# Kernel optimization log

Measured on AMD Instinct MI355X. Metric: run time of the kernel, lower is better.

Reference implementation:

```python
import jax, jax.numpy as jnp
import numpy as np

BETA = 1.0 - 0.01      # 1 - voltage_decay
THRESH = 1.0           # threshold_voltage; theta state is never updated in the
                       # original forward (theta1/theta2 stay at init=0), so the
                       # effective adaptive threshold is THRESH + 0 every step.
ALPHA = 2.0            # snntorch default ATan surrogate alpha

@jax.custom_vjp
def spike_fn(x):
    # Heaviside forward, ATan surrogate backward (snntorch default spike_grad)
    return (x > 0).astype(x.dtype)

def _spike_fwd(x):
    return (x > 0).astype(x.dtype), x

def _spike_bwd(x, g):
    return (g * (ALPHA / 2.0) / (1.0 + (jnp.pi / 2.0 * ALPHA * x) ** 2),)

spike_fn.defvjp(_spike_fwd, _spike_bwd)

def setup_inputs() -> dict:
    key = jax.random.key(0)
    k0, k1, k2 = jax.random.split(key, 3)
    B, T, D, H, A = 128, 32, 6400, 1000, 4
    x = jax.random.normal(k0, (B, T, D), jnp.float32)
    W1 = jax.random.normal(k1, (H, D), jnp.float32) * (1.0 / np.sqrt(D))
    b1 = jnp.zeros((H,), jnp.float32)
    W2 = jax.random.normal(k2, (A, H), jnp.float32) * (1.0 / np.sqrt(H))
    b2 = jnp.zeros((A,), jnp.float32)
    return {"x": x, "W1": W1, "b1": b1, "W2": W2, "b2": b2}

def _lif_step(mem, cur, thr):
    # snntorch Leaky, reset_mechanism='zero':
    #   reset based on PREVIOUS mem crossing threshold (detached),
    #   zeroes the whole new state (leaked mem + input) on reset step.
    reset = jax.lax.stop_gradient((mem > thr).astype(mem.dtype))
    mem_new = (BETA * mem + cur) * (1.0 - reset)
    spk = spike_fn(mem_new - thr)
    return spk, mem_new

def _snn_forward(x, W1, b1, W2, b2):
    B, T, _ = x.shape
    H, A = W1.shape[0], W2.shape[0]

    def step(carry, cur):
        mem1, mem2 = carry
        h1 = cur @ W1.T + b1                 # [B,H]
        spk1, mem1 = _lif_step(mem1, h1, THRESH)
        h2 = spk1 @ W2.T + b2                # [B,A]
        spk2, mem2 = _lif_step(mem2, h2, THRESH)
        return (mem1, mem2), spk2

    init = (jnp.zeros((B, H), x.dtype), jnp.zeros((B, A), x.dtype))
    xt = jnp.swapaxes(x, 0, 1)               # [T,B,D]
    _, spk2_rec = jax.lax.scan(step, init, xt)
    return jnp.swapaxes(spk2_rec, 0, 1)      # [B,T,A]

def reference(x, W1, b1, W2, b2):
    return _snn_forward(x, W1, b1, W2, b2)
```

## Files before the change

kernel.cpp:

```cpp
#include <hip/hip_runtime.h>
#include <hip/hip_bf16.h>

constexpr int Bn = 128;
constexpr int Tn = 32;
constexpr int Dn = 6400;
constexpr int Hn = 1000;
constexpr int An = 4;
constexpr int Mn = Bn * Tn;
constexpr int Npad = 1024;

constexpr int KS = Dn / 32;
constexpr int MC = Mn / 16;
constexpr int NC = Npad / 16;

typedef _Float16 half8 __attribute__((ext_vector_type(8)));
typedef _Float16 half4 __attribute__((ext_vector_type(4)));
typedef float floatx4 __attribute__((ext_vector_type(4)));

constexpr size_t H1_BYTES  = (size_t)Mn * Hn * 4;
constexpr size_t XS_BYTES  = (size_t)Mn * Dn * 2;
constexpr size_t WSp_BYTES = (size_t)Npad * Dn * 2;
constexpr size_t WS_R7     = H1_BYTES + 2 * XS_BYTES + 2 * WSp_BYTES;
constexpr size_t WS_SPLITK = 2 * H1_BYTES + 2 * XS_BYTES + 2 * WSp_BYTES;
constexpr size_t WS_SK3    = 3 * H1_BYTES + 2 * XS_BYTES + 2 * WSp_BYTES;

__device__ __forceinline__ void async16(const void* g, void* l) {
    __builtin_amdgcn_global_load_lds(
        (const __attribute__((address_space(1))) void*)g,
        (__attribute__((address_space(3))) void*)l, 16, 0, 0);
}

__global__ __launch_bounds__(256)
void cvt2(const float* __restrict__ X, const float* __restrict__ W1,
          _Float16* __restrict__ Xh, _Float16* __restrict__ Xl,
          _Float16* __restrict__ Wh, _Float16* __restrict__ Wl)
{
    constexpr int LD2 = 264;
    __shared__ __align__(16) _Float16 hiS[16][LD2];
    __shared__ __align__(16) _Float16 loS[16][LD2];

    const int tid = threadIdx.x;
    const int lane = tid & 63;
    const int w = tid >> 6;
    const int bx = blockIdx.x;

    const float* src;
    _Float16 *dh, *dl;
    int c4, ks0, crow, nrows;
    if (bx < 256 * 25) {
        c4 = bx & 255; ks0 = (bx >> 8) * 8;
        src = X; dh = Xh; dl = Xl; crow = MC; nrows = 16;
    } else {
        const int b2 = bx - 256 * 25;
        c4 = b2 & 63; ks0 = (b2 >> 6) * 8;
        src = W1; dh = Wh; dl = Wl; crow = NC; nrows = Hn - c4 * 16;
    }

#pragma unroll
    for (int j = 0; j < 4; ++j) {
        const int row = w * 4 + j;
        float4 v = make_float4(0.f, 0.f, 0.f, 0.f);
        if (row < nrows)
            v = *(const float4*)(src + (size_t)(c4 * 16 + row) * Dn + ks0 * 32 + lane * 4);
        half4 hi, lo;
        const float vx = v.x * 16.0f, vy = v.y * 16.0f,
                    vz = v.z * 16.0f, vw = v.w * 16.0f;
        hi[0] = (_Float16)vx; lo[0] = (_Float16)(vx - (float)hi[0]);
        hi[1] = (_Float16)vy; lo[1] = (_Float16)(vy - (float)hi[1]);
        hi[2] = (_Float16)vz; lo[2] = (_Float16)(vz - (float)hi[2]);
        hi[3] = (_Float16)vw; lo[3] = (_Float16)(vw - (float)hi[3]);
        *(half4*)&hiS[row][lane * 4] = hi;
        *(half4*)&loS[row][lane * 4] = lo;
    }
    __syncthreads();

    const int lr = lane & 15, lg = lane >> 4;
#pragma unroll
    for (int q = 0; q < 2; ++q) {
        const int ks = w * 2 + q;
        const size_t cbase = ((size_t)(ks0 + ks) * crow + c4) * 512;
        const half8 h = *(const half8*)&hiS[lr][ks * 32 + lg * 8];
        const half8 l = *(const half8*)&loS[lr][ks * 32 + lg * 8];
        *(half8*)(dh + cbase + lane * 8) = h;
        *(half8*)(dl + cbase + lane * 8) = l;
    }
}

__global__ __launch_bounds__(256, 3)
void gemm_sk3(const _Float16* __restrict__ Xh, const _Float16* __restrict__ Xl,
              const _Float16* __restrict__ Wh, const _Float16* __restrict__ Wl,
              float* __restrict__ H1)
{
    __shared__ __align__(16) _Float16 S[3][16][512];

    const int tid = threadIdx.x;
    const int lane = tid & 63;
    const int w = tid >> 6;
    const int bid = blockIdx.x;
    const int kh = bid % 3;
    const int nbmb = bid / 3;
    const int nb = nbmb & 7;
    const int mb = nbmb >> 3;
    const int bm8 = mb * 8;
    const int bn8 = nb * 8;
    const int wm = w & 1;
    const int wn = w >> 1;
    const int ks0 = kh * 67;
    const int NIT = (kh == 2) ? 66 : 67;

    auto issueA = [&](int ks, int buf) {
        _Float16* base = &S[buf][0][0];
#pragma unroll
        for (int r = 0; r < 2; ++r) {
            const int i = w * 2 + r;
            const size_t ga = ((size_t)(ks * MC + bm8 + i)) * 512 + lane * 8;
            async16(Xh + ga, base + (0 + i) * 512);
            async16(Xl + ga, base + (8 + i) * 512);
        }
    };

    const _Float16* bhp = Wh + ((size_t)(ks0 * NC + bn8 + wn * 4)) * 512 + lane * 8;
    const _Float16* blp = Wl + ((size_t)(ks0 * NC + bn8 + wn * 4)) * 512 + lane * 8;
    constexpr size_t BSTEP = (size_t)NC * 512;

    floatx4 acc[4][4] = {};

    issueA(ks0 + 0, 0);
    issueA(ks0 + 1, 1);

#define SK3_BODY(IT, BUF, BUFN)                                                 \
    {                                                                           \
        asm volatile("s_waitcnt vmcnt(4)" ::: "memory");                        \
        __builtin_amdgcn_sched_barrier(0);                                      \
        __builtin_amdgcn_s_barrier();                                           \
        __builtin_amdgcn_sched_barrier(0);                                      \
        half8 bh[4], bl[4];                                                     \
        {                                                                       \
            const size_t bo = (size_t)(IT) * BSTEP;                             \
            _Pragma("unroll")                                                   \
            for (int nt = 0; nt < 4; ++nt) {                                    \
                bh[nt] = *(const half8*)(bhp + bo + nt * 512);                  \
                bl[nt] = *(const half8*)(blp + bo + nt * 512);                  \
            }                                                                   \
        }                                                                       \
        __builtin_amdgcn_sched_barrier(0);                                      \
        if ((IT) + 2 < NIT) issueA(ks0 + (IT) + 2, BUFN);                       \
        __builtin_amdgcn_sched_barrier(0);                                      \
        half8 ah[4], al[4];                                                     \
        _Pragma("unroll")                                                       \
        for (int mt = 0; mt < 4; ++mt) {                                        \
            ah[mt] = *(const half8*)&S[BUF][wm * 4 + mt][lane * 8];             \
            al[mt] = *(const half8*)&S[BUF][8 + wm * 4 + mt][lane * 8];         \
        }                                                                       \
        __builtin_amdgcn_s_setprio(1);                                          \
        _Pragma("unroll")                                                       \
        for (int mt = 0; mt < 4; ++mt)                                          \
            _Pragma("unroll")                                                   \
            for (int nt = 0; nt < 4; ++nt)                                      \
                acc[mt][nt] = __builtin_amdgcn_mfma_f32_16x16x32_f16(ah[mt], bh[nt], acc[mt][nt], 0, 0, 0); \
        _Pragma("unroll")                                                       \
        for (int mt = 0; mt < 4; ++mt)                                          \
            _Pragma("unroll")                                                   \
            for (int nt = 0; nt < 4; ++nt)                                      \
                acc[mt][nt] = __builtin_amdgcn_mfma_f32_16x16x32_f16(ah[mt], bl[nt], acc[mt][nt], 0, 0, 0); \
        _Pragma("unroll")                                                       \
        for (int mt = 0; mt < 4; ++mt)                                          \
            _Pragma("unroll")                                                   \
            for (int nt = 0; nt < 4; ++nt)                                      \
                acc[mt][nt] = __builtin_amdgcn_mfma_f32_16x16x32_f16(al[mt], bh[nt], acc[mt][nt], 0, 0, 0); \
        __builtin_amdgcn_s_setprio(0);                                          \
    }

    int it = 0;
    for (; it + 3 <= NIT; it += 3) {
        SK3_BODY(it + 0, 0, 2);
        SK3_BODY(it + 1, 1, 0);
        SK3_BODY(it + 2, 2, 1);
    }
    if (it < NIT) {
        SK3_BODY(it, 0, 2);
    }
#undef SK3_BODY

    float* H1o = H1 + (size_t)kh * ((size_t)Mn * Hn);
    const int fr = lane & 15;
    const int fq = lane >> 4;
#pragma unroll
    for (int nt = 0; nt < 4; ++nt) {
        const int n = nb * 128 + wn * 64 + nt * 16 + fr;
        if (n >= Hn) continue;
#pragma unroll
        for (int mt = 0; mt < 4; ++mt) {
            const int m = mb * 128 + wm * 64 + mt * 16 + fq * 4;
#pragma unroll
            for (int r = 0; r < 4; ++r)
                H1o[(size_t)(m + r) * Hn + n] = acc[mt][nt][r] * (1.0f / 256.0f);
        }
    }
}

__global__ __launch_bounds__(256, 2)
void gemm_sk2(const _Float16* __restrict__ Xh, const _Float16* __restrict__ Xl,
              const _Float16* __restrict__ Wh, const _Float16* __restrict__ Wl,
              float* __restrict__ H1)
{
    __shared__ __align__(16) _Float16 S[4][16][512];

    const int tid = threadIdx.x;
    const int lane = tid & 63;
    const int w = tid >> 6;
    const int kh = blockIdx.x & 1;
    const int nb = (blockIdx.x >> 1) & 7;
    const int mb = blockIdx.x >> 4;
    const int bm8 = mb * 8;
    const int bn8 = nb * 8;
    const int wm = w & 1;
    const int wn = w >> 1;
    const int ks0 = kh * (KS / 2);
    constexpr int NIT = KS / 2;

    auto issueA = [&](int ks, int buf) {
        _Float16* base = &S[buf][0][0];
#pragma unroll
        for (int r = 0; r < 2; ++r) {
            const int i = w * 2 + r;
            const size_t ga = ((size_t)(ks * MC + bm8 + i)) * 512 + lane * 8;
            async16(Xh + ga, base + (0 + i) * 512);
            async16(Xl + ga, base + (8 + i) * 512);
        }
    };

    const _Float16* bhp = Wh + ((size_t)(ks0 * NC + bn8 + wn * 4)) * 512 + lane * 8;
    const _Float16* blp = Wl + ((size_t)(ks0 * NC + bn8 + wn * 4)) * 512 + lane * 8;
    constexpr size_t BSTEP = (size_t)NC * 512;

    floatx4 acc[4][4] = {};

    issueA(ks0 + 0, 0);
    issueA(ks0 + 1, 1);

#define SK2_BODY(IT, BUF)                                                       \
    {                                                                           \
        asm volatile("s_waitcnt vmcnt(4)" ::: "memory");                        \
        __builtin_amdgcn_sched_barrier(0);                                      \
        __builtin_amdgcn_s_barrier();                                           \
        __builtin_amdgcn_sched_barrier(0);                                      \
        half8 bh[4], bl[4];                                                     \
        {                                                                       \
            const size_t bo = (size_t)(IT) * BSTEP;                             \
            _Pragma("unroll")                                                   \
            for (int nt = 0; nt < 4; ++nt) {                                    \
                bh[nt] = *(const half8*)(bhp + bo + nt * 512);                  \
                bl[nt] = *(const half8*)(blp + bo + nt * 512);                  \
            }                                                                   \
        }                                                                       \
        __builtin_amdgcn_sched_barrier(0);                                      \
        if ((IT) + 2 < NIT) issueA(ks0 + (IT) + 2, ((IT) + 2) & 3);             \
        __builtin_amdgcn_sched_barrier(0);                                      \
        half8 ah[4], al[4];                                                     \
        _Pragma("unroll")                                                       \
        for (int mt = 0; mt < 4; ++mt) {                                        \
            ah[mt] = *(const half8*)&S[BUF][wm * 4 + mt][lane * 8];             \
            al[mt] = *(const half8*)&S[BUF][8 + wm * 4 + mt][lane * 8];         \
        }                                                                       \
        _Pragma("unroll")                                                       \
        for (int mt = 0; mt < 4; ++mt)                                          \
            _Pragma("unroll")                                                   \
            for (int nt = 0; nt < 4; ++nt)                                      \
                acc[mt][nt] = __builtin_amdgcn_mfma_f32_16x16x32_f16(ah[mt], bh[nt], acc[mt][nt], 0, 0, 0); \
        _Pragma("unroll")                                                       \
        for (int mt = 0; mt < 4; ++mt)                                          \
            _Pragma("unroll")                                                   \
            for (int nt = 0; nt < 4; ++nt)                                      \
                acc[mt][nt] = __builtin_amdgcn_mfma_f32_16x16x32_f16(ah[mt], bl[nt], acc[mt][nt], 0, 0, 0); \
        _Pragma("unroll")                                                       \
        for (int mt = 0; mt < 4; ++mt)                                          \
            _Pragma("unroll")                                                   \
            for (int nt = 0; nt < 4; ++nt)                                      \
                acc[mt][nt] = __builtin_amdgcn_mfma_f32_16x16x32_f16(al[mt], bh[nt], acc[mt][nt], 0, 0, 0); \
    }

    for (int it = 0; it < NIT; it += 4) {
        SK2_BODY(it + 0, 0);
        SK2_BODY(it + 1, 1);
        SK2_BODY(it + 2, 2);
        SK2_BODY(it + 3, 3);
    }
#undef SK2_BODY

    float* H1o = H1 + (size_t)kh * ((size_t)Mn * Hn);
    const int fr = lane & 15;
    const int fq = lane >> 4;
#pragma unroll
    for (int nt = 0; nt < 4; ++nt) {
        const int n = nb * 128 + wn * 64 + nt * 16 + fr;
        if (n >= Hn) continue;
#pragma unroll
        for (int mt = 0; mt < 4; ++mt) {
            const int m = mb * 128 + wm * 64 + mt * 16 + fq * 4;
#pragma unroll
            for (int r = 0; r < 4; ++r)
                H1o[(size_t)(m + r) * Hn + n] = acc[mt][nt][r] * (1.0f / 256.0f);
        }
    }
}

constexpr int AH = 0;
constexpr int AL = 8 * 512;
constexpr int BH = 16 * 512;
constexpr int BL = 20 * 512;
constexpr int BUFSZ = 24 * 512;

__global__ __launch_bounds__(256, 2)
void gemm_frag2(const _Float16* __restrict__ Xh, const _Float16* __restrict__ Xl,
                const _Float16* __restrict__ Wh, const _Float16* __restrict__ Wl,
                float* __restrict__ H1)
{
    __shared__ __align__(16) _Float16 S[2 * BUFSZ];

    const int tid = threadIdx.x;
    const int lane = tid & 63;
    const int w = tid >> 6;
    const int nb = blockIdx.x & 15;
    const int mb = blockIdx.x >> 4;
    const int bm4 = mb * 8;
    const int bn4 = nb * 4;
    const int wm = w & 1;
    const int wn = w >> 1;

    auto issue = [&](int ks, int buf) {
        _Float16* base = &S[buf * BUFSZ];
#pragma unroll
        for (int r = 0; r < 2; ++r) {
            const int i = w * 2 + r;
            const size_t ga = ((size_t)(ks * MC + bm4 + i)) * 512 + lane * 8;
            async16(Xh + ga, base + AH + i * 512);
            async16(Xl + ga, base + AL + i * 512);
        }
        const size_t gb = ((size_t)(ks * NC + bn4 + w)) * 512 + lane * 8;
        async16(Wh + gb, base + BH + w * 512);
        async16(Wl + gb, base + BL + w * 512);
    };

    floatx4 acc0[4][2] = {};
    floatx4 acc1[4][2] = {};

    issue(0, 0);
    for (int it = 0; it < KS; ++it) {
        const int buf = it & 1;
        __syncthreads();
        if (it + 1 < KS) issue(it + 1, buf ^ 1);

        const _Float16* base = &S[buf * BUFSZ];
        half8 ah[4], al[4], bh[2], bl[2];
#pragma unroll
        for (int mt = 0; mt < 4; ++mt) {
            ah[mt] = *(const half8*)(base + AH + (wm * 4 + mt) * 512 + lane * 8);
            al[mt] = *(const half8*)(base + AL + (wm * 4 + mt) * 512 + lane * 8);
        }
#pragma unroll
        for (int nt = 0; nt < 2; ++nt) {
            bh[nt] = *(const half8*)(base + BH + (wn * 2 + nt) * 512 + lane * 8);
            bl[nt] = *(const half8*)(base + BL + (wn * 2 + nt) * 512 + lane * 8);
        }
#pragma unroll
        for (int mt = 0; mt < 4; ++mt)
#pragma unroll
            for (int nt = 0; nt < 2; ++nt) {
                acc0[mt][nt] = __builtin_amdgcn_mfma_f32_16x16x32_f16(ah[mt], bh[nt], acc0[mt][nt], 0, 0, 0);
                acc1[mt][nt] = __builtin_amdgcn_mfma_f32_16x16x32_f16(ah[mt], bl[nt], acc1[mt][nt], 0, 0, 0);
                acc1[mt][nt] = __builtin_amdgcn_mfma_f32_16x16x32_f16(al[mt], bh[nt], acc1[mt][nt], 0, 0, 0);
            }
    }

    const int fr = lane & 15;
    const int fq = lane >> 4;
#pragma unroll
    for (int nt = 0; nt < 2; ++nt) {
        const int n = nb * 64 + wn * 32 + nt * 16 + fr;
        if (n >= Hn) continue;
#pragma unroll
        for (int mt = 0; mt < 4; ++mt) {
            const int m = mb * 128 + wm * 64 + mt * 16 + fq * 4;
#pragma unroll
            for (int r = 0; r < 4; ++r)
                H1[(size_t)(m + r) * Hn + n] =
                    (acc0[mt][nt][r] + acc1[mt][nt][r]) * (1.0f / 256.0f);
        }
    }
}

__global__ __launch_bounds__(256, 4)
void gemm_fb(const float* __restrict__ X, const float* __restrict__ W1,
             float* __restrict__ H1)
{
    constexpr int K = Dn;
    constexpr int LD = 72;
    __shared__ __align__(16) _Float16 As[2][64][LD];
    __shared__ __align__(16) _Float16 Bs[2][64][LD];

    const int tid = threadIdx.x;
    const int bm = blockIdx.x * 64;
    const int bn = blockIdx.y * 64;
    const int lane = tid & 63;
    const int wid = tid >> 6;
    const int wm = (wid & 1) * 32;
    const int wn = (wid >> 1) * 32;
    const int fr = lane & 15;
    const int fq = lane >> 4;

    const int row0 = tid >> 3;
    const int row1 = (tid + 256) >> 3;
    const int k8_0 = (tid & 7) * 8;

    float4 rx[2][2], rw[2][2];
    const float zero4[4] = {0.f, 0.f, 0.f, 0.f};

    auto load_tiles = [&](int k0) {
        rx[0][0] = *(const float4*)(X + (size_t)(bm + row0) * K + k0 + k8_0);
        rx[0][1] = *(const float4*)(X + (size_t)(bm + row0) * K + k0 + k8_0 + 4);
        rx[1][0] = *(const float4*)(X + (size_t)(bm + row1) * K + k0 + k8_0);
        rx[1][1] = *(const float4*)(X + (size_t)(bm + row1) * K + k0 + k8_0 + 4);
        const int n0 = bn + row0, n1 = bn + row1;
        if (n0 < Hn) {
            rw[0][0] = *(const float4*)(W1 + (size_t)n0 * K + k0 + k8_0);
            rw[0][1] = *(const float4*)(W1 + (size_t)n0 * K + k0 + k8_0 + 4);
        } else { rw[0][0] = *(const float4*)zero4; rw[0][1] = *(const float4*)zero4; }
        if (n1 < Hn) {
            rw[1][0] = *(const float4*)(W1 + (size_t)n1 * K + k0 + k8_0);
            rw[1][1] = *(const float4*)(W1 + (size_t)n1 * K + k0 + k8_0 + 4);
        } else { rw[1][0] = *(const float4*)zero4; rw[1][1] = *(const float4*)zero4; }
    };

    load_tiles(0);
    floatx4 acc0[2][2] = {};
    floatx4 acc1[2][2] = {};

    for (int k0 = 0; k0 < K; k0 += 64) {
#pragma unroll
        for (int p = 0; p < 2; ++p) {
            const int row = p ? row1 : row0;
            float v[8];
            *(float4*)&v[0] = rx[p][0]; *(float4*)&v[4] = rx[p][1];
            half8 hi, lo;
#pragma unroll
            for (int j = 0; j < 8; ++j) {
                hi[j] = (_Float16)v[j];
                lo[j] = (_Float16)((v[j] - (float)hi[j]) * 4096.0f);
            }
            *(half8*)&As[0][row][k8_0] = hi;
            *(half8*)&As[1][row][k8_0] = lo;

            *(float4*)&v[0] = rw[p][0]; *(float4*)&v[4] = rw[p][1];
#pragma unroll
            for (int j = 0; j < 8; ++j) {
                hi[j] = (_Float16)v[j];
                lo[j] = (_Float16)((v[j] - (float)hi[j]) * 4096.0f);
            }
            *(half8*)&Bs[0][row][k8_0] = hi;
            *(half8*)&Bs[1][row][k8_0] = lo;
        }
        __syncthreads();
        if (k0 + 64 < K) load_tiles(k0 + 64);

#pragma unroll
        for (int c = 0; c < 2; ++c) {
            half8 ahi[2], alo[2], bhi[2], blo[2];
#pragma unroll
            for (int mt = 0; mt < 2; ++mt) {
                ahi[mt] = *(const half8*)&As[0][wm + mt * 16 + fr][c * 32 + fq * 8];
                alo[mt] = *(const half8*)&As[1][wm + mt * 16 + fr][c * 32 + fq * 8];
            }
#pragma unroll
            for (int nt = 0; nt < 2; ++nt) {
                bhi[nt] = *(const half8*)&Bs[0][wn + nt * 16 + fr][c * 32 + fq * 8];
                blo[nt] = *(const half8*)&Bs[1][wn + nt * 16 + fr][c * 32 + fq * 8];
            }
#pragma unroll
            for (int mt = 0; mt < 2; ++mt)
#pragma unroll
                for (int nt = 0; nt < 2; ++nt) {
                    acc0[mt][nt] = __builtin_amdgcn_mfma_f32_16x16x32_f16(ahi[mt], bhi[nt], acc0[mt][nt], 0, 0, 0);
                    acc1[mt][nt] = __builtin_amdgcn_mfma_f32_16x16x32_f16(ahi[mt], blo[nt], acc1[mt][nt], 0, 0, 0);
                    acc1[mt][nt] = __builtin_amdgcn_mfma_f32_16x16x32_f16(alo[mt], bhi[nt], acc1[mt][nt], 0, 0, 0);
                }
        }
        __syncthreads();
    }

#pragma unroll
    for (int nt = 0; nt < 2; ++nt) {
        const int n = bn + wn + nt * 16 + fr;
        if (n >= Hn) continue;
#pragma unroll
        for (int mt = 0; mt < 2; ++mt) {
            const int m = bm + wm + mt * 16 + fq * 4;
#pragma unroll
            for (int r = 0; r < 4; ++r)
                H1[(size_t)(m + r) * Hn + n] =
                    acc0[mt][nt][r] + acc1[mt][nt][r] * (1.0f / 4096.0f);
        }
    }
}

__global__ __launch_bounds__(1024)
void snn_scan(const float* __restrict__ H1, const float* __restrict__ b1,
              const float* __restrict__ W2, const float* __restrict__ b2,
              float* __restrict__ out, int split)
{
    const int b = blockIdx.x;
    const int tid = threadIdx.x;
    const int lane = tid & 63;
    const int wid = tid >> 6;
    const bool act = (tid < Hn);
    constexpr size_t MH = (size_t)Mn * Hn;

    __shared__ float w2s[1024][5];
    __shared__ unsigned smask[1024];
    __shared__ float h2s[Tn][An];

#pragma unroll
    for (int a = 0; a < An; ++a)
        w2s[tid][a] = act ? W2[a * Hn + tid] : 0.f;

    const float b1v = act ? b1[tid] : 0.f;

    float cur[Tn];
#pragma unroll
    for (int t = 0; t < Tn; ++t) {
        const size_t idx = ((size_t)b * Tn + t) * Hn + tid;
        float c = act ? H1[idx] : 0.f;
        if (act)
            for (int s = 1; s <= split; ++s) c += H1[idx + (size_t)s * MH];
        cur[t] = c + b1v;
    }

    unsigned mask = 0;
    float mem1 = 0.f;
#pragma unroll
    for (int t = 0; t < Tn; ++t) {
        const float reset = (mem1 > 1.0f) ? 1.0f : 0.0f;
        mem1 = (0.99f * mem1 + cur[t]) * (1.0f - reset);
        if (mem1 > 1.0f) mask |= (1u << t);
    }
    smask[tid] = act ? mask : 0u;
    __syncthreads();

#pragma unroll
    for (int tt = 0; tt < 2; ++tt) {
        const int t = wid * 2 + tt;
        float p[An] = {0.f, 0.f, 0.f, 0.f};
        for (int h = lane; h < 1024; h += 64) {
            const float g = (smask[h] >> t) & 1u ? 1.0f : 0.0f;
#pragma unroll
            for (int a = 0; a < An; ++a) p[a] += g * w2s[h][a];
        }
#pragma unroll
        for (int off = 32; off > 0; off >>= 1)
#pragma unroll
            for (int a = 0; a < An; ++a) p[a] += __shfl_down(p[a], off, 64);
        if (lane == 0) {
#pragma unroll
            for (int a = 0; a < An; ++a) h2s[t][a] = p[a];
        }
    }
    __syncthreads();

    if (tid < An) {
        const float bias = b2[tid];
        float mem2 = 0.f;
#pragma unroll
        for (int t = 0; t < Tn; ++t) {
            const float h2 = h2s[t][tid] + bias;
            const float reset = (mem2 > 1.0f) ? 1.0f : 0.0f;
            mem2 = (0.99f * mem2 + h2) * (1.0f - reset);
            out[((size_t)b * Tn + t) * An + tid] = (mem2 > 1.0f) ? 1.0f : 0.0f;
        }
    }
}

extern "C" void kernel_launch(void* const* d_in, const int* in_sizes, int n_in,
                              void* d_out, int out_size, void* d_ws, size_t ws_size,
                              hipStream_t stream) {
    const float* x  = (const float*)d_in[0];
    const float* W1 = (const float*)d_in[1];
    const float* b1 = (const float*)d_in[2];
    const float* W2 = (const float*)d_in[3];
    const float* b2 = (const float*)d_in[4];
    float* out = (float*)d_out;

    char* ws = (char*)d_ws;
    float* H1 = (float*)ws;

    if (ws_size >= WS_SK3) {
        _Float16* Xh = (_Float16*)(ws + 3 * H1_BYTES);
        _Float16* Xl = (_Float16*)(ws + 3 * H1_BYTES + XS_BYTES);
        _Float16* Wh = (_Float16*)(ws + 3 * H1_BYTES + 2 * XS_BYTES);
        _Float16* Wl = (_Float16*)(ws + 3 * H1_BYTES + 2 * XS_BYTES + WSp_BYTES);

        cvt2<<<256 * 25 + 64 * 25, 256, 0, stream>>>(x, W1, Xh, Xl, Wh, Wl);
        gemm_sk3<<<768, 256, 0, stream>>>(Xh, Xl, Wh, Wl, H1);
        snn_scan<<<Bn, 1024, 0, stream>>>(H1, b1, W2, b2, out, 2);
    } else if (ws_size >= WS_SPLITK) {
        _Float16* Xh = (_Float16*)(ws + 2 * H1_BYTES);
        _Float16* Xl = (_Float16*)(ws + 2 * H1_BYTES + XS_BYTES);
        _Float16* Wh = (_Float16*)(ws + 2 * H1_BYTES + 2 * XS_BYTES);
        _Float16* Wl = (_Float16*)(ws + 2 * H1_BYTES + 2 * XS_BYTES + WSp_BYTES);

        cvt2<<<256 * 25 + 64 * 25, 256, 0, stream>>>(x, W1, Xh, Xl, Wh, Wl);
        gemm_sk2<<<512, 256, 0, stream>>>(Xh, Xl, Wh, Wl, H1);
        snn_scan<<<Bn, 1024, 0, stream>>>(H1, b1, W2, b2, out, 1);
    } else if (ws_size >= WS_R7) {
        _Float16* Xh = (_Float16*)(ws + H1_BYTES);
        _Float16* Xl = (_Float16*)(ws + H1_BYTES + XS_BYTES);
        _Float16* Wh = (_Float16*)(ws + H1_BYTES + 2 * XS_BYTES);
        _Float16* Wl = (_Float16*)(ws + H1_BYTES + 2 * XS_BYTES + WSp_BYTES);

        cvt2<<<256 * 25 + 64 * 25, 256, 0, stream>>>(x, W1, Xh, Xl, Wh, Wl);
        gemm_frag2<<<512, 256, 0, stream>>>(Xh, Xl, Wh, Wl, H1);
        snn_scan<<<Bn, 1024, 0, stream>>>(H1, b1, W2, b2, out, 0);
    } else {
        dim3 grid(Mn / 64, (Hn + 63) / 64);
        gemm_fb<<<grid, 256, 0, stream>>>(x, W1, H1);
        snn_scan<<<Bn, 1024, 0, stream>>>(H1, b1, W2, b2, out, 0);
    }
}
```

Baseline: 378.6 us.

## Replace 3-way split-K GEMM with 512-thread phased-pipeline 2-way split-K GEMM

Drops the 3-way split-K GEMM path. The 2-way split-K path now runs a new 512-thread kernel with a 256-row M tile and a 4-deep LDS ring. The k-step is broken into four per-M-tile phases: A fragments are double-buffered in registers, B fragments are prefetched one k-step ahead into alternating register sets, and the vmcnt wait happens only once per k-step. The aim is to hide LDS and global load latency behind MFMAs and to halve the partial-sum traffic into the scan. The costs are one block per CU (256 blocks), higher register pressure, and fewer blocks for latency hiding.

After: 367.1 us. -3.0%, faster.

```diff
diff --git a/kernel.cpp b/kernel.cpp
--- a/kernel.cpp
+++ b/kernel.cpp
@@ -22,7 +22,6 @@
 constexpr size_t WSp_BYTES = (size_t)Npad * Dn * 2;
 constexpr size_t WS_R7     = H1_BYTES + 2 * XS_BYTES + 2 * WSp_BYTES;
 constexpr size_t WS_SPLITK = 2 * H1_BYTES + 2 * XS_BYTES + 2 * WSp_BYTES;
-constexpr size_t WS_SK3    = 3 * H1_BYTES + 2 * XS_BYTES + 2 * WSp_BYTES;
 
 __device__ __forceinline__ void async16(const void* g, void* l) {
     __builtin_amdgcn_global_load_lds(
@@ -86,36 +85,34 @@
     }
 }
 
-__global__ __launch_bounds__(256, 3)
-void gemm_sk3(const _Float16* __restrict__ Xh, const _Float16* __restrict__ Xl,
-              const _Float16* __restrict__ Wh, const _Float16* __restrict__ Wl,
-              float* __restrict__ H1)
+__global__ __launch_bounds__(512, 1)
+void gemm_ph(const _Float16* __restrict__ Xh, const _Float16* __restrict__ Xl,
+             const _Float16* __restrict__ Wh, const _Float16* __restrict__ Wl,
+             float* __restrict__ H1)
 {
-    __shared__ __align__(16) _Float16 S[3][16][512];
+    __shared__ __align__(16) _Float16 S[4][32][512];
 
     const int tid = threadIdx.x;
     const int lane = tid & 63;
     const int w = tid >> 6;
-    const int bid = blockIdx.x;
-    const int kh = bid % 3;
-    const int nbmb = bid / 3;
-    const int nb = nbmb & 7;
-    const int mb = nbmb >> 3;
-    const int bm8 = mb * 8;
+    const int kh = blockIdx.x & 1;
+    const int nb = (blockIdx.x >> 1) & 7;
+    const int mb = blockIdx.x >> 4;
+    const int bm16 = mb * 16;
     const int bn8 = nb * 8;
-    const int wm = w & 1;
-    const int wn = w >> 1;
-    const int ks0 = kh * 67;
-    const int NIT = (kh == 2) ? 66 : 67;
+    const int wm = w >> 1;
+    const int wn = w & 1;
+    const int ks0 = kh * (KS / 2);
+    constexpr int NIT = KS / 2;
 
     auto issueA = [&](int ks, int buf) {
         _Float16* base = &S[buf][0][0];
 #pragma unroll
         for (int r = 0; r < 2; ++r) {
             const int i = w * 2 + r;
-            const size_t ga = ((size_t)(ks * MC + bm8 + i)) * 512 + lane * 8;
+            const size_t ga = ((size_t)(ks * MC + bm16 + i)) * 512 + lane * 8;
             async16(Xh + ga, base + (0 + i) * 512);
-            async16(Xl + ga, base + (8 + i) * 512);
+            async16(Xl + ga, base + (16 + i) * 512);
         }
     };
 
@@ -125,62 +122,78 @@
 
     floatx4 acc[4][4] = {};
 
+    half8 bh0[4], bl0[4], bh1[4], bl1[4];
+    half8 aaH, aaL, abH, abL;
+
     issueA(ks0 + 0, 0);
     issueA(ks0 + 1, 1);
-
-#define SK3_BODY(IT, BUF, BUFN)                                                 \
+#pragma unroll
+    for (int nt = 0; nt < 4; ++nt) bh0[nt] = *(const half8*)(bhp + nt * 512);
+#pragma unroll
+    for (int nt = 0; nt < 4; ++nt) bl0[nt] = *(const half8*)(blp + nt * 512);
+    asm volatile("s_waitcnt vmcnt(12)" ::: "memory");
+    __builtin_amdgcn_sched_barrier(0);
+    __builtin_amdgcn_s_barrier();
+    __builtin_amdgcn_sched_barrier(0);
+    aaH = *(const half8*)&S[0][wm * 4 + 0][lane * 8];
+    aaL = *(const half8*)&S[0][16 + wm * 4 + 0][lane * 8];
+
+#define PH(IT, BUF, P, ACURH, ACURL, ANXH, ANXL, BCH, BCL, BNH, BNL, DO_VM)     \
     {                                                                           \
-        asm volatile("s_waitcnt vmcnt(4)" ::: "memory");                        \
+        if (DO_VM) asm volatile("s_waitcnt vmcnt(12)" ::: "memory");            \
         __builtin_amdgcn_sched_barrier(0);                                      \
         __builtin_amdgcn_s_barrier();                                           \
         __builtin_amdgcn_sched_barrier(0);                                      \
-        half8 bh[4], bl[4];                                                     \
-        {                                                                       \
-            const size_t bo = (size_t)(IT) * BSTEP;                             \
+        if ((P) == 0 && (IT) + 1 < NIT) {                                       \
+            const size_t bo = (size_t)((IT) + 1) * BSTEP;                       \
             _Pragma("unroll")                                                   \
-            for (int nt = 0; nt < 4; ++nt) {                                    \
-                bh[nt] = *(const half8*)(bhp + bo + nt * 512);                  \
-                bl[nt] = *(const half8*)(blp + bo + nt * 512);                  \
+            for (int nt2 = 0; nt2 < 4; ++nt2)                                   \
+                BNH[nt2] = *(const half8*)(bhp + bo + nt2 * 512);               \
+        }                                                                       \
+        if ((P) == 1) {                                                         \
+            if ((IT) + 1 < NIT) {                                               \
+                const size_t bo = (size_t)((IT) + 1) * BSTEP;                   \
+                _Pragma("unroll")                                               \
+                for (int nt2 = 0; nt2 < 4; ++nt2)                               \
+                    BNL[nt2] = *(const half8*)(blp + bo + nt2 * 512);           \
             }                                                                   \
+            if ((IT) + 2 < NIT) issueA(ks0 + (IT) + 2, ((IT) + 2) & 3);         \
+        }                                                                       \
+        if ((P) < 3) {                                                          \
+            ANXH = *(const half8*)&S[BUF][wm * 4 + (P) + 1][lane * 8];          \
+            ANXL = *(const half8*)&S[BUF][16 + wm * 4 + (P) + 1][lane * 8];     \
+        } else if ((IT) + 1 < NIT) {                                            \
+            ANXH = *(const half8*)&S[((IT) + 1) & 3][wm * 4 + 0][lane * 8];     \
+            ANXL = *(const half8*)&S[((IT) + 1) & 3][16 + wm * 4 + 0][lane * 8];\
         }                                                                       \
         __builtin_amdgcn_sched_barrier(0);                                      \
-        if ((IT) + 2 < NIT) issueA(ks0 + (IT) + 2, BUFN);                       \
-        __builtin_amdgcn_sched_barrier(0);                                      \
-        half8 ah[4], al[4];                                                     \
-        _Pragma("unroll")                                                       \
-        for (int mt = 0; mt < 4; ++mt) {                                        \
-            ah[mt] = *(const half8*)&S[BUF][wm * 4 + mt][lane * 8];             \
-            al[mt] = *(const half8*)&S[BUF][8 + wm * 4 + mt][lane * 8];         \
-        }                                                                       \
         __builtin_amdgcn_s_setprio(1);                                          \
         _Pragma("unroll")                                                       \
-        for (int mt = 0; mt < 4; ++mt)                                          \
-            _Pragma("unroll")                                                   \
-            for (int nt = 0; nt < 4; ++nt)                                      \
-                acc[mt][nt] = __builtin_amdgcn_mfma_f32_16x16x32_f16(ah[mt], bh[nt], acc[mt][nt], 0, 0, 0); \
+        for (int nt2 = 0; nt2 < 4; ++nt2)                                       \
+            acc[P][nt2] = __builtin_amdgcn_mfma_f32_16x16x32_f16(ACURH, BCH[nt2], acc[P][nt2], 0, 0, 0); \
         _Pragma("unroll")                                                       \
-        for (int mt = 0; mt < 4; ++mt)                                          \
-            _Pragma("unroll")                                                   \
-            for (int nt = 0; nt < 4; ++nt)                                      \
-                acc[mt][nt] = __builtin_amdgcn_mfma_f32_16x16x32_f16(ah[mt], bl[nt], acc[mt][nt], 0, 0, 0); \
+        for (int nt2 = 0; nt2 < 4; ++nt2)                                       \
+            acc[P][nt2] = __builtin_amdgcn_mfma_f32_16x16x32_f16(ACURH, BCL[nt2], acc[P][nt2], 0, 0, 0); \
         _Pragma("unroll")                                                       \
-        for (int mt = 0; mt < 4; ++mt)                                          \
-            _Pragma("unroll")                                                   \
-            for (int nt = 0; nt < 4; ++nt)                                      \
-                acc[mt][nt] = __builtin_amdgcn_mfma_f32_16x16x32_f16(al[mt], bh[nt], acc[mt][nt], 0, 0, 0); \
+        for (int nt2 = 0; nt2 < 4; ++nt2)                                       \
+            acc[P][nt2] = __builtin_amdgcn_mfma_f32_16x16x32_f16(ACURL, BCH[nt2], acc[P][nt2], 0, 0, 0); \
         __builtin_amdgcn_s_setprio(0);                                          \
     }
 
-    int it = 0;
-    for (; it + 3 <= NIT; it += 3) {
-        SK3_BODY(it + 0, 0, 2);
-        SK3_BODY(it + 1, 1, 0);
-        SK3_BODY(it + 2, 2, 1);
-    }
-    if (it < NIT) {
-        SK3_BODY(it, 0, 2);
-    }
-#undef SK3_BODY
+#define CHUNK(IT, BUF, BCH, BCL, BNH, BNL)                                      \
+    PH(IT, BUF, 0, aaH, aaL, abH, abL, BCH, BCL, BNH, BNL, 0)                   \
+    PH(IT, BUF, 1, abH, abL, aaH, aaL, BCH, BCL, BNH, BNL, 0)                   \
+    PH(IT, BUF, 2, aaH, aaL, abH, abL, BCH, BCL, BNH, BNL, 0)                   \
+    PH(IT, BUF, 3, abH, abL, aaH, aaL, BCH, BCL, BNH, BNL, 1)
+
+    for (int it = 0; it < NIT; it += 4) {
+        CHUNK(it + 0, 0, bh0, bl0, bh1, bl1);
+        CHUNK(it + 1, 1, bh1, bl1, bh0, bl0);
+        CHUNK(it + 2, 2, bh0, bl0, bh1, bl1);
+        CHUNK(it + 3, 3, bh1, bl1, bh0, bl0);
+    }
+#undef CHUNK
+#undef PH
 
     float* H1o = H1 + (size_t)kh * ((size_t)Mn * Hn);
     const int fr = lane & 15;
@@ -191,7 +204,7 @@
         if (n >= Hn) continue;
 #pragma unroll
         for (int mt = 0; mt < 4; ++mt) {
-            const int m = mb * 128 + wm * 64 + mt * 16 + fq * 4;
+            const int m = mb * 256 + wm * 64 + mt * 16 + fq * 4;
 #pragma unroll
             for (int r = 0; r < 4; ++r)
                 H1o[(size_t)(m + r) * Hn + n] = acc[mt][nt][r] * (1.0f / 256.0f);
@@ -592,23 +605,14 @@
     char* ws = (char*)d_ws;
     float* H1 = (float*)ws;
 
-    if (ws_size >= WS_SK3) {
-        _Float16* Xh = (_Float16*)(ws + 3 * H1_BYTES);
-        _Float16* Xl = (_Float16*)(ws + 3 * H1_BYTES + XS_BYTES);
-        _Float16* Wh = (_Float16*)(ws + 3 * H1_BYTES + 2 * XS_BYTES);
-        _Float16* Wl = (_Float16*)(ws + 3 * H1_BYTES + 2 * XS_BYTES + WSp_BYTES);
-
-        cvt2<<<256 * 25 + 64 * 25, 256, 0, stream>>>(x, W1, Xh, Xl, Wh, Wl);
-        gemm_sk3<<<768, 256, 0, stream>>>(Xh, Xl, Wh, Wl, H1);
-        snn_scan<<<Bn, 1024, 0, stream>>>(H1, b1, W2, b2, out, 2);
-    } else if (ws_size >= WS_SPLITK) {
+    if (ws_size >= WS_SPLITK) {
         _Float16* Xh = (_Float16*)(ws + 2 * H1_BYTES);
         _Float16* Xl = (_Float16*)(ws + 2 * H1_BYTES + XS_BYTES);
         _Float16* Wh = (_Float16*)(ws + 2 * H1_BYTES + 2 * XS_BYTES);
         _Float16* Wl = (_Float16*)(ws + 2 * H1_BYTES + 2 * XS_BYTES + WSp_BYTES);
 
         cvt2<<<256 * 25 + 64 * 25, 256, 0, stream>>>(x, W1, Xh, Xl, Wh, Wl);
-        gemm_sk2<<<512, 256, 0, stream>>>(Xh, Xl, Wh, Wl, H1);
+        gemm_ph<<<256, 512, 0, stream>>>(Xh, Xl, Wh, Wl, H1);
         snn_scan<<<Bn, 1024, 0, stream>>>(H1, b1, W2, b2, out, 1);
     } else if (ws_size >= WS_R7) {
         _Float16* Xh = (_Float16*)(ws + H1_BYTES);
```
